# Kernel optimization log

Measured on AMD Instinct MI355X. Metric: run time of the kernel, lower is better.

The kernel has to match this reference:

```python
import jax, jax.numpy as jnp
import numpy as np

NUM_CHUNKS = 8
TOP_K = 2
IN_F = 4096
HID_F = 4096
OUT_F = 4096
B = 4096


def setup_inputs() -> dict:
    key = jax.random.key(0)
    k = jax.random.split(key, 5)
    cin = IN_F // NUM_CHUNKS    # 512
    cout = HID_F // NUM_CHUNKS  # 512
    s_in = 1.0 / np.sqrt(cin)
    s_fin = 1.0 / np.sqrt(cout * TOP_K)
    return {
        "x": jax.random.normal(k[0], (B, IN_F), dtype=jnp.float32),
        # stacked chunk-expert Linear params: y = x @ W + b
        "W_chunks": jax.random.uniform(k[1], (NUM_CHUNKS, cin, cout), jnp.float32, -s_in, s_in),
        "b_chunks": jax.random.uniform(k[2], (NUM_CHUNKS, cout), jnp.float32, -s_in, s_in),
        "W_final": jax.random.uniform(k[3], (cout * TOP_K, OUT_F), jnp.float32, -s_fin, s_fin),
        "b_final": jax.random.uniform(k[4], (OUT_F,), jnp.float32, -s_fin, s_fin),
    }


def reference(x, W_chunks, b_chunks, W_final, b_final):
    Bsz = x.shape[0]
    # split into chunks along feature dim: (B, num_chunks, chunk_in)
    xr = x.reshape(Bsz, NUM_CHUNKS, -1)
    # per-chunk activity = mean(|chunk|) over the whole batch (matches torch .abs().mean())
    activities = jnp.mean(jnp.abs(xr), axis=(0, 2))  # (num_chunks,)
    _, topk_idx = jax.lax.top_k(activities, TOP_K)    # descending, like torch.topk
    # gather selected chunks and their expert weights, run small GEMMs
    x_sel = xr[:, topk_idx, :]                        # (B, k, chunk_in)
    h = jnp.einsum('bkc,kcd->bkd', x_sel, W_chunks[topk_idx]) + b_chunks[topk_idx]
    h = h.reshape(Bsz, -1)                            # concat along feature dim
    out = h @ W_final + b_final                       # (B, out_features)
    return out
```

## Files before the change

kernel.cpp:

```cpp
#include <hip/hip_runtime.h>


typedef __bf16 bf16x8_t __attribute__((ext_vector_type(8)));
typedef float  f32x4_t  __attribute__((ext_vector_type(4)));

__device__ inline unsigned short f2bf(float f) {
    __bf16 b = (__bf16)f;
    return __builtin_bit_cast(unsigned short, b);
}

__device__ inline void stage_glds(const unsigned short* gtile, int stride, int row0,
                                  unsigned short* lds, int lane) {
    const int r8 = lane >> 3;
    const int gg = (lane & 7) ^ r8;
    const unsigned short* gp = gtile + (size_t)(row0 + r8) * stride + gg * 8;
    unsigned short* lp = lds + row0 * 64;
    __builtin_amdgcn_global_load_lds((const __attribute__((address_space(1))) void*)gp,
                                     (__attribute__((address_space(3))) void*)lp,
                                     16, 0, 0);
}

__device__ inline bf16x8_t ldsfrag(const unsigned short* Ls, int row, int kb) {
    return *(const bf16x8_t*)(Ls + row * 64 + (((kb >> 3) ^ (row & 7)) * 8));
}

__device__ inline void stage32(const unsigned short* gtile, int row0,
                               unsigned short* lds, int lane) {
    const int r  = lane >> 2;
    const int gg = (lane & 3) ^ ((r >> 1) & 3);
    const unsigned short* gp = gtile + (size_t)(row0 + r) * 1024 + gg * 8;
    unsigned short* lp = lds + row0 * 32;
    __builtin_amdgcn_global_load_lds((const __attribute__((address_space(1))) void*)gp,
                                     (__attribute__((address_space(3))) void*)lp,
                                     16, 0, 0);
}

__device__ inline bf16x8_t ldsfrag32(const unsigned short* Ls, int row, int kb) {
    return *(const bf16x8_t*)(Ls + row * 32 + ((((kb >> 3) ^ ((row >> 1) & 3))) * 8));
}

__global__ void fused_prep_kernel(const float* __restrict__ x, const float* __restrict__ Wc,
                                  const float* __restrict__ Wf, float* __restrict__ part,
                                  unsigned short* __restrict__ wct, unsigned short* __restrict__ wft) {
    const int b = blockIdx.x;
    const int tid = threadIdx.x;

    if (b < 512) {
        const int chunk = b & 7;
        const int rg = b >> 3;
        const int colf4 = tid & 127;
        const int rsub = tid >> 7;
        const float4* base = (const float4*)x + (size_t)chunk * 128 + colf4;
        float s = 0.f;
        #pragma unroll 4
        for (int i = 0; i < 32; ++i) {
            int row = rg * 64 + i * 2 + rsub;
            float4 v = base[(size_t)row * 1024];
            s += fabsf(v.x) + fabsf(v.y) + fabsf(v.z) + fabsf(v.w);
        }
        #pragma unroll
        for (int off = 32; off > 0; off >>= 1) s += __shfl_down(s, off, 64);
        __shared__ float wsum[4];
        if ((tid & 63) == 0) wsum[tid >> 6] = s;
        __syncthreads();
        if (tid == 0) part[chunk * 64 + rg] = wsum[0] + wsum[1] + wsum[2] + wsum[3];
        return;
    }

    __shared__ float tile[32][33];
    const int tx = tid & 31, ty = tid >> 5;
    const float* src; unsigned short* dst; int R, C, cb, rb;
    int jj = b - 512;
    if (jj < 4096) {
        src = Wf; dst = wft; R = 1024; C = 4096;
        cb = (jj & 127) * 32; rb = (jj >> 7) * 32;
    } else {
        jj -= 4096;
        int c = jj >> 8, t = jj & 255;
        src = Wc + (size_t)c * 262144;
        dst = wct + (size_t)c * 262144;
        R = 512; C = 512;
        cb = (t & 15) * 32; rb = (t >> 4) * 32;
    }
    #pragma unroll
    for (int i = 0; i < 4; ++i)
        tile[ty + i * 8][tx] = src[(size_t)(rb + ty + i * 8) * C + cb + tx];
    __syncthreads();
    #pragma unroll
    for (int i = 0; i < 4; ++i)
        dst[(size_t)(cb + ty + i * 8) * R + rb + tx] = f2bf(tile[tx][ty + i * 8]);
}

__global__ __launch_bounds__(256, 4)
void gemm1_kernel(const float* __restrict__ x, const unsigned short* __restrict__ wct,
                  const float* __restrict__ bc, const float* __restrict__ part,
                  unsigned short* __restrict__ h) {
    __shared__ __align__(16) unsigned char lds_raw[24576];
    unsigned short* As = (unsigned short*)lds_raw;
    unsigned short* Bs = (unsigned short*)(lds_raw + 8192);

    const int tid = threadIdx.x;
    const int wave = tid >> 6;
    const int lane = tid & 63;

    {
        float* sred = (float*)lds_raw;
        sred[tid] = part[tid];
        sred[tid + 256] = part[tid + 256];
        __syncthreads();
        float* act8 = (float*)(lds_raw + 2048);
        if (tid < 8) {
            float a = 0.f;
            #pragma unroll
            for (int k = 0; k < 64; ++k) a += sred[tid * 64 + k];
            act8[tid] = a;
        }
        __syncthreads();
    }
    int sel0, sel1;
    {
        const float* act8 = (const float*)(lds_raw + 2048);
        float v0 = -1e30f, v1 = -1e30f; int b0 = 0, b1 = 0;
        #pragma unroll
        for (int i = 0; i < 8; ++i) {
            float v = act8[i];
            if (v > v0) { v1 = v0; b1 = b0; v0 = v; b0 = i; }
            else if (v > v1) { v1 = v; b1 = i; }
        }
        sel0 = b0; sel1 = b1;
    }
    __syncthreads();

    const int z = blockIdx.z;
    const int idxz = z ? sel1 : sel0;
    const int m0 = blockIdx.x * 64;
    const int n0 = blockIdx.y * 128;
    const int wm = (wave >> 1) * 32;
    const int wn = (wave & 1) * 64;
    const int rl = lane & 15;
    const int quad = lane >> 4;

    const float* xtile = x + (size_t)m0 * 4096 + idxz * 512;
    const unsigned short* Btile = wct + (size_t)idxz * 262144 + (size_t)n0 * 512;

    f32x4_t acc[2][4] = {};
    const int ar = tid >> 2;
    const int aq = tid & 3;

    for (int k0 = 0; k0 < 512; k0 += 64) {
        #pragma unroll
        for (int s = wave; s < 16; s += 4)
            stage_glds(Btile + k0, 512, s * 8, Bs, lane);
        const float* gr = xtile + (size_t)ar * 4096 + k0;
        #pragma unroll
        for (int j = 0; j < 2; ++j) {
            int gg = aq * 2 + j;
            float4 a = *(const float4*)(gr + gg * 8);
            float4 c = *(const float4*)(gr + gg * 8 + 4);
            bf16x8_t v;
            v[0] = (__bf16)a.x; v[1] = (__bf16)a.y; v[2] = (__bf16)a.z; v[3] = (__bf16)a.w;
            v[4] = (__bf16)c.x; v[5] = (__bf16)c.y; v[6] = (__bf16)c.z; v[7] = (__bf16)c.w;
            *(bf16x8_t*)(As + ar * 64 + ((gg ^ (ar & 7)) * 8)) = v;
        }
        __syncthreads();
        #pragma unroll
        for (int kq = 0; kq < 2; ++kq) {
            const int kb = kq * 32 + quad * 8;
            bf16x8_t af[2], bfr[4];
            #pragma unroll
            for (int i = 0; i < 2; ++i) af[i]  = ldsfrag(As, wm + i * 16 + rl, kb);
            #pragma unroll
            for (int i = 0; i < 4; ++i) bfr[i] = ldsfrag(Bs, wn + i * 16 + rl, kb);
            #pragma unroll
            for (int mi = 0; mi < 2; ++mi)
                #pragma unroll
                for (int ni = 0; ni < 4; ++ni)
                    acc[mi][ni] = __builtin_amdgcn_mfma_f32_16x16x32_bf16(af[mi], bfr[ni], acc[mi][ni], 0, 0, 0);
        }
        __syncthreads();
    }

    const int row_l = quad * 4;
    const float* bias = bc + (size_t)idxz * 512;
    #pragma unroll
    for (int ni = 0; ni < 4; ++ni) {
        int col = n0 + wn + ni * 16 + rl;
        float bv = bias[col];
        #pragma unroll
        for (int mi = 0; mi < 2; ++mi) {
            #pragma unroll
            for (int j = 0; j < 4; ++j) {
                int row = m0 + wm + mi * 16 + row_l + j;
                h[(size_t)row * 1024 + z * 512 + col] = f2bf(acc[mi][ni][j] + bv);
            }
        }
    }
}

__global__ __launch_bounds__(512, 2)
void gemm2_kernel(const unsigned short* __restrict__ h, const unsigned short* __restrict__ wft,
                  const float* __restrict__ bfin, float* __restrict__ out) {
    __shared__ __align__(16) unsigned short lds[65536];

    const int tid  = threadIdx.x;
    const int wv   = tid >> 6;
    const int lane = tid & 63;
    const int m0 = blockIdx.x * 256;
    const int n0 = blockIdx.y * 256;
    const int wmo = (wv >> 2) * 128;
    const int wno = (wv & 3) * 64;
    const int rl   = lane & 15;
    const int quad = lane >> 4;
    const int kb   = quad * 8;
    const int srow = wv * 32;

    const unsigned short* Atile = h   + (size_t)m0 * 1024;
    const unsigned short* Btile = wft + (size_t)n0 * 1024;

    f32x4_t acc[8][4] = {};

    #pragma unroll
    for (int p = 0; p < 3; ++p) {
        unsigned short* As_n = lds + p * 16384;
        unsigned short* Bs_n = As_n + 8192;
        stage32(Atile + p * 32, srow,      As_n, lane);
        stage32(Atile + p * 32, srow + 16, As_n, lane);
        stage32(Btile + p * 32, srow,      Bs_n, lane);
        stage32(Btile + p * 32, srow + 16, Bs_n, lane);
    }

    #pragma unroll 4
    for (int t = 0; t < 32; ++t) {
        __builtin_amdgcn_sched_barrier(0);
        {
            const int tn = (t + 3 < 32) ? (t + 3) : 31;
            unsigned short* As_n = lds + ((t + 3) & 3) * 16384;
            unsigned short* Bs_n = As_n + 8192;
            stage32(Atile + tn * 32, srow,      As_n, lane);
            stage32(Atile + tn * 32, srow + 16, As_n, lane);
            stage32(Btile + tn * 32, srow,      Bs_n, lane);
            stage32(Btile + tn * 32, srow + 16, Bs_n, lane);
        }
        asm volatile("s_waitcnt vmcnt(12)" ::: "memory");
        __builtin_amdgcn_sched_barrier(0);
        __builtin_amdgcn_s_barrier();
        __builtin_amdgcn_sched_barrier(0);

        const unsigned short* As = lds + (t & 3) * 16384;
        const unsigned short* Bs = As + 8192;
        bf16x8_t bfr[4], af[8];
        #pragma unroll
        for (int i = 0; i < 4; ++i) bfr[i] = ldsfrag32(Bs, wno + i * 16 + rl, kb);
        #pragma unroll
        for (int i = 0; i < 8; ++i) af[i]  = ldsfrag32(As, wmo + i * 16 + rl, kb);

        __builtin_amdgcn_s_setprio(1);
        #pragma unroll
        for (int mi = 0; mi < 8; ++mi)
            #pragma unroll
            for (int ni = 0; ni < 4; ++ni)
                acc[mi][ni] = __builtin_amdgcn_mfma_f32_16x16x32_bf16(af[mi], bfr[ni], acc[mi][ni], 0, 0, 0);
        __builtin_amdgcn_s_setprio(0);
        __builtin_amdgcn_sched_barrier(0);
        __builtin_amdgcn_s_barrier();
    }
    asm volatile("s_waitcnt vmcnt(0)" ::: "memory");

    const int row_l = quad * 4;
    float bv[4];
    #pragma unroll
    for (int ni = 0; ni < 4; ++ni) bv[ni] = bfin[n0 + wno + ni * 16 + rl];
    #pragma unroll
    for (int j = 0; j < 4; ++j) {
        #pragma unroll
        for (int mi = 0; mi < 8; ++mi) {
            int row = m0 + wmo + mi * 16 + row_l + j;
            float* orow = out + (size_t)row * 4096 + n0 + wno + rl;
            #pragma unroll
            for (int ni = 0; ni < 4; ++ni)
                orow[ni * 16] = acc[mi][ni][j] + bv[ni];
        }
    }
}

extern "C" void kernel_launch(void* const* d_in, const int* in_sizes, int n_in,
                              void* d_out, int out_size, void* d_ws, size_t ws_size,
                              hipStream_t stream) {
    const float* x    = (const float*)d_in[0];
    const float* Wc   = (const float*)d_in[1];
    const float* bc   = (const float*)d_in[2];
    const float* Wf   = (const float*)d_in[3];
    const float* bfin = (const float*)d_in[4];
    float* out = (float*)d_out;

    float* part = (float*)d_ws;
    unsigned short* h   = (unsigned short*)((char*)d_ws + 4096);
    unsigned short* wct = h   + (size_t)4096 * 1024;
    unsigned short* wft = wct + (size_t)8 * 512 * 512;

    fused_prep_kernel<<<6656, 256, 0, stream>>>(x, Wc, Wf, part, wct, wft);
    gemm1_kernel<<<dim3(64, 4, 2), 256, 0, stream>>>(x, wct, bc, part, h);
    gemm2_kernel<<<dim3(16, 16, 1), 512, 0, stream>>>(h, wft, bfin, out);
}
```

Before: 184.4 us.

## Restructure GEMM2 pipeline to one barrier with split staging; vectorize GEMM1 and transpose stores

```diff
diff --git a/kernel.cpp b/kernel.cpp
--- a/kernel.cpp
+++ b/kernel.cpp
@@ -3,6 +3,7 @@
 
 typedef __bf16 bf16x8_t __attribute__((ext_vector_type(8)));
 typedef float  f32x4_t  __attribute__((ext_vector_type(4)));
+typedef unsigned short u16x4 __attribute__((ext_vector_type(4)));
 
 __device__ inline unsigned short f2bf(float f) {
     __bf16 b = (__bf16)f;
@@ -86,9 +87,14 @@
     for (int i = 0; i < 4; ++i)
         tile[ty + i * 8][tx] = src[(size_t)(rb + ty + i * 8) * C + cb + tx];
     __syncthreads();
-    #pragma unroll
-    for (int i = 0; i < 4; ++i)
-        dst[(size_t)(cb + ty + i * 8) * R + rb + tx] = f2bf(tile[tx][ty + i * 8]);
+    {
+        const int tx8  = tid & 7;
+        const int ty32 = tid >> 3;
+        u16x4 hv;
+        #pragma unroll
+        for (int j = 0; j < 4; ++j) hv[j] = f2bf(tile[tx8 * 4 + j][ty32]);
+        *(u16x4*)(dst + (size_t)(cb + ty32) * R + rb + tx8 * 4) = hv;
+    }
 }
 
 __global__ __launch_bounds__(256, 4)
@@ -143,7 +149,7 @@
     const float* xtile = x + (size_t)m0 * 4096 + idxz * 512;
     const unsigned short* Btile = wct + (size_t)idxz * 262144 + (size_t)n0 * 512;
 
-    f32x4_t acc[2][4] = {};
+    f32x4_t acc[4][2] = {};
     const int ar = tid >> 2;
     const int aq = tid & 3;
 
@@ -172,27 +178,27 @@
             #pragma unroll
             for (int i = 0; i < 4; ++i) bfr[i] = ldsfrag(Bs, wn + i * 16 + rl, kb);
             #pragma unroll
-            for (int mi = 0; mi < 2; ++mi)
+            for (int ni = 0; ni < 4; ++ni)
                 #pragma unroll
-                for (int ni = 0; ni < 4; ++ni)
-                    acc[mi][ni] = __builtin_amdgcn_mfma_f32_16x16x32_bf16(af[mi], bfr[ni], acc[mi][ni], 0, 0, 0);
-        }
-        __syncthreads();
-    }
-
-    const int row_l = quad * 4;
+                for (int mi = 0; mi < 2; ++mi)
+                    acc[ni][mi] = __builtin_amdgcn_mfma_f32_16x16x32_bf16(bfr[ni], af[mi], acc[ni][mi], 0, 0, 0);
+        }
+        __syncthreads();
+    }
+
     const float* bias = bc + (size_t)idxz * 512;
     #pragma unroll
     for (int ni = 0; ni < 4; ++ni) {
-        int col = n0 + wn + ni * 16 + rl;
-        float bv = bias[col];
+        const int colb = n0 + wn + ni * 16 + quad * 4;
+        f32x4_t bv4 = *(const f32x4_t*)(bias + colb);
         #pragma unroll
         for (int mi = 0; mi < 2; ++mi) {
-            #pragma unroll
-            for (int j = 0; j < 4; ++j) {
-                int row = m0 + wm + mi * 16 + row_l + j;
-                h[(size_t)row * 1024 + z * 512 + col] = f2bf(acc[mi][ni][j] + bv);
-            }
+            int row = m0 + wm + mi * 16 + rl;
+            f32x4_t o = acc[ni][mi] + bv4;
+            u16x4 hv;
+            #pragma unroll
+            for (int j = 0; j < 4; ++j) hv[j] = f2bf(o[j]);
+            *(u16x4*)(h + (size_t)row * 1024 + z * 512 + colb) = hv;
         }
     }
 }
@@ -221,48 +227,53 @@
 
     #pragma unroll
     for (int p = 0; p < 3; ++p) {
-        unsigned short* As_n = lds + p * 16384;
-        unsigned short* Bs_n = As_n + 8192;
-        stage32(Atile + p * 32, srow,      As_n, lane);
-        stage32(Atile + p * 32, srow + 16, As_n, lane);
-        stage32(Btile + p * 32, srow,      Bs_n, lane);
-        stage32(Btile + p * 32, srow + 16, Bs_n, lane);
+        unsigned short* Ap = lds + p * 8192;
+        unsigned short* Bp = lds + 32768 + p * 8192;
+        stage32(Atile + p * 32, srow,      Ap, lane);
+        stage32(Atile + p * 32, srow + 16, Ap, lane);
+        stage32(Btile + p * 32, srow,      Bp, lane);
+        stage32(Btile + p * 32, srow + 16, Bp, lane);
     }
 
     #pragma unroll 4
     for (int t = 0; t < 32; ++t) {
-        __builtin_amdgcn_sched_barrier(0);
-        {
-            const int tn = (t + 3 < 32) ? (t + 3) : 31;
-            unsigned short* As_n = lds + ((t + 3) & 3) * 16384;
-            unsigned short* Bs_n = As_n + 8192;
-            stage32(Atile + tn * 32, srow,      As_n, lane);
-            stage32(Atile + tn * 32, srow + 16, As_n, lane);
-            stage32(Btile + tn * 32, srow,      Bs_n, lane);
-            stage32(Btile + tn * 32, srow + 16, Bs_n, lane);
-        }
-        asm volatile("s_waitcnt vmcnt(12)" ::: "memory");
-        __builtin_amdgcn_sched_barrier(0);
+        const unsigned short* Ac = lds + (t & 3) * 8192;
+        const unsigned short* Bc = lds + 32768 + (t & 3) * 8192;
+        const int tn = (t + 3 < 32) ? t + 3 : 31;
+        unsigned short* An = lds + ((t + 3) & 3) * 8192;
+        unsigned short* Bn = lds + 32768 + ((t + 3) & 3) * 8192;
+
+        asm volatile("s_waitcnt vmcnt(8)" ::: "memory");
         __builtin_amdgcn_s_barrier();
         __builtin_amdgcn_sched_barrier(0);
 
-        const unsigned short* As = lds + (t & 3) * 16384;
-        const unsigned short* Bs = As + 8192;
-        bf16x8_t bfr[4], af[8];
-        #pragma unroll
-        for (int i = 0; i < 4; ++i) bfr[i] = ldsfrag32(Bs, wno + i * 16 + rl, kb);
-        #pragma unroll
-        for (int i = 0; i < 8; ++i) af[i]  = ldsfrag32(As, wmo + i * 16 + rl, kb);
-
+        bf16x8_t bf[4], af[4];
+        #pragma unroll
+        for (int i = 0; i < 4; ++i) bf[i] = ldsfrag32(Bc, wno + i * 16 + rl, kb);
+        #pragma unroll
+        for (int i = 0; i < 4; ++i) af[i] = ldsfrag32(Ac, wmo + i * 16 + rl, kb);
+        stage32(Atile + tn * 32, srow,      An, lane);
+        stage32(Atile + tn * 32, srow + 16, An, lane);
         __builtin_amdgcn_s_setprio(1);
         #pragma unroll
-        for (int mi = 0; mi < 8; ++mi)
+        for (int mi = 0; mi < 4; ++mi)
             #pragma unroll
             for (int ni = 0; ni < 4; ++ni)
-                acc[mi][ni] = __builtin_amdgcn_mfma_f32_16x16x32_bf16(af[mi], bfr[ni], acc[mi][ni], 0, 0, 0);
+                acc[mi][ni] = __builtin_amdgcn_mfma_f32_16x16x32_bf16(af[mi], bf[ni], acc[mi][ni], 0, 0, 0);
         __builtin_amdgcn_s_setprio(0);
-        __builtin_amdgcn_sched_barrier(0);
-        __builtin_amdgcn_s_barrier();
+
+        bf16x8_t ag[4];
+        #pragma unroll
+        for (int i = 0; i < 4; ++i) ag[i] = ldsfrag32(Ac, wmo + 64 + i * 16 + rl, kb);
+        stage32(Btile + tn * 32, srow,      Bn, lane);
+        stage32(Btile + tn * 32, srow + 16, Bn, lane);
+        __builtin_amdgcn_s_setprio(1);
+        #pragma unroll
+        for (int mi = 0; mi < 4; ++mi)
+            #pragma unroll
+            for (int ni = 0; ni < 4; ++ni)
+                acc[4 + mi][ni] = __builtin_amdgcn_mfma_f32_16x16x32_bf16(ag[mi], bf[ni], acc[4 + mi][ni], 0, 0, 0);
+        __builtin_amdgcn_s_setprio(0);
     }
     asm volatile("s_waitcnt vmcnt(0)" ::: "memory");
 
```

After: 185.3 us. About the same (+0.5%).
